# Performance work log

Measured on AMD Instinct MI355X. Metric: run time of the kernel, lower is better.

Reference implementation:

```python
import jax, jax.numpy as jnp
import numpy as np

PATCH_SIZE = 3
CHANNELS = 1
SIGMA_RAW = 0.5
SIGMA_EFF = SIGMA_RAW * PATCH_SIZE ** 2  # sigma * patch_size**2 as in __init__


def setup_inputs() -> dict:
    key = jax.random.key(0)
    kx, ky = jax.random.split(key)
    N, C, H, W = 64, CHANNELS, 64, 64
    x = jax.random.normal(kx, (N, C, H, W), dtype=jnp.float32)
    y = jax.random.normal(ky, (N, C, H, W), dtype=jnp.float32)
    return {"x": x, "y": y}


def _pairwise_patch_distance(A, B):
    # A: (N_A, C, H, W), B: (N_B, C, H, W)
    N_A, C, H, W = A.shape
    N_B = B.shape[0]
    # broadcast pairwise squared pixel diffs: (N_A, N_B, C, H, W)
    pixel_diff = (A[:, None] - B[None]) ** 2
    kern = jnp.ones((1, C, PATCH_SIZE, PATCH_SIZE), dtype=A.dtype)  # OIHW
    d = jax.lax.conv_general_dilated(
        pixel_diff.reshape(N_A * N_B, C, H, W), kern,
        window_strides=(1, 1), padding='VALID',
        dimension_numbers=('NCHW', 'OIHW', 'NCHW'))
    H_new, W_new = d.shape[-2], d.shape[-1]
    return d.reshape(N_A, N_B, H_new, W_new)


def _gaussian_kernel(D):
    return jnp.exp(-D / (2.0 * SIGMA_EFF ** 2))


def _off_mean(K):
    # K: (N, N, h, w); mean over all off-diagonal (i != j) entries
    N, _, h, w = K.shape
    mask = ~jnp.eye(N, dtype=bool)
    total = jnp.sum(jnp.where(mask[:, :, None, None], K, jnp.zeros((), K.dtype)))
    count = (N * (N - 1)) * h * w
    return total / count


def reference(x, y):
    K_xx = _gaussian_kernel(_pairwise_patch_distance(x, x))
    K_xy = _gaussian_kernel(_pairwise_patch_distance(x, y))
    K_yy = _gaussian_kernel(_pairwise_patch_distance(y, y))
    return _off_mean(K_xx) - 2.0 * jnp.mean(K_xy) + _off_mean(K_yy)
```

## Files before the change

### kernel.cpp

```cpp
#include <hip/hip_runtime.h>


typedef __attribute__((ext_vector_type(8))) short short8v;
typedef __attribute__((ext_vector_type(4))) float f32x4;

#define NPOS 3844
#define SIM  196

#if __has_builtin(__builtin_amdgcn_exp2f)
#define EXP2F(v) __builtin_amdgcn_exp2f(v)
#else
#define EXP2F(v) __expf((v) * 0.69314718055994530942f)
#endif

template<int CTRL>
__device__ __forceinline__ float dpp0_f(float v) {
    int r = __builtin_amdgcn_update_dpp(0, __float_as_int(v), CTRL, 0xf, 0xf, true);
    return __int_as_float(r);
}
template<int CTRL, int RM>
__device__ __forceinline__ float dppm_f(float v) {
    int r = __builtin_amdgcn_update_dpp(0, __float_as_int(v), CTRL, RM, 0xf, true);
    return __int_as_float(r);
}
__device__ __forceinline__ float wave_reduce_f(float v) {
    v += dpp0_f<0x111>(v);
    v += dpp0_f<0x112>(v);
    v += dpp0_f<0x114>(v);
    v += dpp0_f<0x118>(v);
    v += dppm_f<0x142, 0xa>(v);
    v += dppm_f<0x143, 0xc>(v);
    return v;
}

__device__ __forceinline__ unsigned int bf16rne(float f) {
    unsigned int u = __float_as_uint(f);
    return (u + 0x7fffu + ((u >> 16) & 1u)) >> 16;
}

__global__ __launch_bounds__(512) void mmd_fused_kernel(
    const float* __restrict__ x, const float* __restrict__ y,
    float* __restrict__ part)
{
    const int t = threadIdx.x, wid = t >> 6, lane = t & 63;
    const int p  = blockIdx.x >> 3;
    const int qg = blockIdx.x & 7;
    const int q  = qg * 8 + wid;

    __shared__ unsigned short stg[128 * SIM];
    __shared__ float pre[8][128];

    #pragma unroll
    for (int u = 0; u < 3; ++u) {
        #pragma unroll
        for (int k = 0; k < 4; ++k) {
            int it = t + k * 512;
            int n = it >> 4, cg = it & 15;
            const float* img = (n < 64) ? (x + n * 4096) : (y + (n - 64) * 4096);
            float4 v = *reinterpret_cast<const float4*>(img + (p + u) * 64 + cg * 4);
            uint2 pk;
            pk.x = bf16rne(v.x) | (bf16rne(v.y) << 16);
            pk.y = bf16rne(v.z) | (bf16rne(v.w) << 16);
            *reinterpret_cast<uint2*>(&stg[n * SIM + u * 64 + cg * 4]) = pk;
        }
    }
    __syncthreads();

    const int r = lane & 15, kg = lane >> 4;
    short8v frag[8];
    #pragma unroll
    for (int g = 0; g < 8; ++g) {
        const unsigned short* bp = &stg[(g * 16 + r) * SIM];
        short8v f = {0, 0, 0, 0, 0, 0, 0, 0};
        if (kg == 0) {
            f[0] = (short)bp[q];
            f[1] = (short)bp[q + 1];
            f[2] = (short)bp[q + 2];
            f[3] = (short)bp[64 + q];
            f[4] = (short)bp[64 + q + 1];
            f[5] = (short)bp[64 + q + 2];
            f[6] = (short)bp[128 + q];
            f[7] = (short)bp[128 + q + 1];
        } else if (kg == 1) {
            f[0] = (short)bp[128 + q + 2];
        }
        frag[g] = f;
    }

    const float NS   = -1.0f / (40.5f * 0.69314718055994530942f);
    const float M2NS = -2.0f * NS;
    const f32x4 zf = {0.f, 0.f, 0.f, 0.f};

    f32x4 accd[8];
    #pragma unroll
    for (int g = 0; g < 8; ++g)
        accd[g] = __builtin_amdgcn_mfma_f32_16x16x32_bf16(frag[g], frag[g], zf, 0, 0, 0);

    const bool holder = ((lane >> 2) & 3) == kg;
    #pragma unroll
    for (int g = 0; g < 8; ++g) {
        float lo = (lane & 1) ? accd[g][1] : accd[g][0];
        float hi = (lane & 1) ? accd[g][3] : accd[g][2];
        float v  = (lane & 2) ? hi : lo;
        if (holder) pre[wid][g * 16 + (lane & 15)] = NS * v;
    }
    __syncthreads();

    float pa[8][4], pb[8];
    #pragma unroll
    for (int g = 0; g < 8; ++g) {
        const float* pp = &pre[wid][g * 16 + kg * 4];
        pa[g][0] = pp[0]; pa[g][1] = pp[1]; pa[g][2] = pp[2]; pa[g][3] = pp[3];
        pb[g] = pre[wid][g * 16 + (lane & 15)];
    }

    float acc_diag = 0.f, acc_same = 0.f, acc_cross = 0.f;

    #pragma unroll
    for (int g = 0; g < 8; ++g)
        #pragma unroll
        for (int m = 0; m < 4; ++m)
            acc_diag += EXP2F(fmaf(accd[g][m], M2NS, pa[g][m] + pb[g]));

    #pragma unroll
    for (int ti = 1; ti < 8; ++ti)
        #pragma unroll
        for (int tj = 0; tj < ti; ++tj) {
            f32x4 c4 = __builtin_amdgcn_mfma_f32_16x16x32_bf16(frag[ti], frag[tj], zf, 0, 0, 0);
            float e = 0.f;
            #pragma unroll
            for (int m = 0; m < 4; ++m)
                e += EXP2F(fmaf(c4[m], M2NS, pa[ti][m] + pb[tj]));
            if (ti >= 4 && tj < 4) acc_cross += e; else acc_same += e;
        }

    acc_diag  = wave_reduce_f(acc_diag);
    acc_same  = wave_reduce_f(acc_same);
    acc_cross = wave_reduce_f(acc_cross);
    if (lane == 63 && q < 62) {
        const int pid = p * 62 + q;
        part[pid]        = acc_diag;
        part[4096 + pid] = acc_same;
        part[8192 + pid] = acc_cross;
    }
}

__global__ __launch_bounds__(1024) void mmd_final_kernel(
    const float* __restrict__ part, float* __restrict__ out)
{
    const int t = threadIdx.x;
    double sd = 0.0, ss = 0.0, sc = 0.0;
    for (int e = t; e < NPOS; e += 1024) {
        sd += (double)part[e];
        ss += (double)part[4096 + e];
        sc += (double)part[8192 + e];
    }
    #pragma unroll
    for (int off = 32; off > 0; off >>= 1) {
        sd += __shfl_xor(sd, off);
        ss += __shfl_xor(ss, off);
        sc += __shfl_xor(sc, off);
    }
    __shared__ double w[3][16];
    const int lane = t & 63, wd = t >> 6;
    if (lane == 0) { w[0][wd] = sd; w[1][wd] = ss; w[2][wd] = sc; }
    __syncthreads();
    if (t == 0) {
        double Sd = 0.0, Ss = 0.0, Sc = 0.0;
        #pragma unroll
        for (int k = 0; k < 16; ++k) { Sd += w[0][k]; Ss += w[1][k]; Sc += w[2][k]; }
        double S_off = (Sd - 128.0 * (double)NPOS) + 2.0 * Ss;
        const double cnt_off = 64.0 * 63.0 * 62.0 * 62.0;
        const double cnt_all = 64.0 * 64.0 * 62.0 * 62.0;
        out[0] = (float)(S_off / cnt_off - 2.0 * Sc / cnt_all);
    }
}

extern "C" void kernel_launch(void* const* d_in, const int* in_sizes, int n_in,
                              void* d_out, int out_size, void* d_ws, size_t ws_size,
                              hipStream_t stream) {
    const float* x = (const float*)d_in[0];
    const float* y = (const float*)d_in[1];
    float* out  = (float*)d_out;
    float* part = (float*)d_ws;

    mmd_fused_kernel<<<62 * 8, 512, 0, stream>>>(x, y, part);
    mmd_final_kernel<<<1, 1024, 0, stream>>>(part, out);
}
```

Measured before the change: 19.11 us.

## Stage narrow per-block windows and prebuilt patch records for vectorized fragment loads

Each block now covers 4 output columns instead of 8, with 256 threads and twice as many blocks. It stages only a 3x8 column window per image instead of three full rows. A second pass packs each 9-pixel patch into a 16-byte record plus a trailing element, so MFMA fragments load with one vector LDS read instead of eight scalar reads. The intent is to cut global loads, shared memory footprint and scalar LDS traffic, and to raise occupancy, at the cost of an extra repacking pass and barrier.

```diff
diff --git a/kernel.cpp b/kernel.cpp
--- a/kernel.cpp
+++ b/kernel.cpp
@@ -5,7 +5,7 @@
 typedef __attribute__((ext_vector_type(4))) float f32x4;
 
 #define NPOS 3844
-#define SIM  196
+#define WSTR 26
 
 #if __has_builtin(__builtin_amdgcn_exp2f)
 #define EXP2F(v) __builtin_amdgcn_exp2f(v)
@@ -32,37 +32,63 @@
     v += dppm_f<0x143, 0xc>(v);
     return v;
 }
-
 __device__ __forceinline__ unsigned int bf16rne(float f) {
     unsigned int u = __float_as_uint(f);
     return (u + 0x7fffu + ((u >> 16) & 1u)) >> 16;
 }
 
-__global__ __launch_bounds__(512) void mmd_fused_kernel(
+__global__ __launch_bounds__(256) void mmd_fused_kernel(
     const float* __restrict__ x, const float* __restrict__ y,
     float* __restrict__ part)
 {
     const int t = threadIdx.x, wid = t >> 6, lane = t & 63;
-    const int p  = blockIdx.x >> 3;
-    const int qg = blockIdx.x & 7;
-    const int q  = qg * 8 + wid;
-
-    __shared__ unsigned short stg[128 * SIM];
-    __shared__ float pre[8][128];
-
-    #pragma unroll
-    for (int u = 0; u < 3; ++u) {
-        #pragma unroll
-        for (int k = 0; k < 4; ++k) {
-            int it = t + k * 512;
-            int n = it >> 4, cg = it & 15;
+    const int p  = blockIdx.x >> 4;
+    const int qg = blockIdx.x & 15;
+    const int q  = qg * 4 + wid;
+
+    __shared__ unsigned short win[128 * WSTR];
+    __shared__ unsigned short rec[4 * 128 * 8];
+    __shared__ unsigned short rec8[4 * 128];
+    __shared__ float pre[4][128];
+
+    {
+        const int cg1 = (qg < 15) ? qg + 1 : 15;
+        #pragma unroll
+        for (int k = 0; k < 3; ++k) {
+            int it = t + k * 256;
+            int n = it / 6, rem = it % 6;
+            int u = rem >> 1, cg = rem & 1;
             const float* img = (n < 64) ? (x + n * 4096) : (y + (n - 64) * 4096);
-            float4 v = *reinterpret_cast<const float4*>(img + (p + u) * 64 + cg * 4);
-            uint2 pk;
-            pk.x = bf16rne(v.x) | (bf16rne(v.y) << 16);
-            pk.y = bf16rne(v.z) | (bf16rne(v.w) << 16);
-            *reinterpret_cast<uint2*>(&stg[n * SIM + u * 64 + cg * 4]) = pk;
+            float4 v = *reinterpret_cast<const float4*>(
+                img + (p + u) * 64 + ((cg ? cg1 : qg) << 2));
+            unsigned int d0 = bf16rne(v.x) | (bf16rne(v.y) << 16);
+            unsigned int d1 = bf16rne(v.z) | (bf16rne(v.w) << 16);
+            unsigned int* w32 = reinterpret_cast<unsigned int*>(
+                &win[n * WSTR + u * 8 + cg * 4]);
+            w32[0] = d0; w32[1] = d1;
         }
+    }
+    __syncthreads();
+
+    #pragma unroll
+    for (int k = 0; k < 2; ++k) {
+        int rid = t + k * 256;
+        int ql = rid >> 7, n = rid & 127;
+        const unsigned short* wp = &win[n * WSTR + ql];
+        unsigned short b[9];
+        #pragma unroll
+        for (int u = 0; u < 3; ++u) {
+            b[u * 3 + 0] = wp[u * 8 + 0];
+            b[u * 3 + 1] = wp[u * 8 + 1];
+            b[u * 3 + 2] = wp[u * 8 + 2];
+        }
+        uint4 pk;
+        pk.x = b[0] | ((unsigned)b[1] << 16);
+        pk.y = b[2] | ((unsigned)b[3] << 16);
+        pk.z = b[4] | ((unsigned)b[5] << 16);
+        pk.w = b[6] | ((unsigned)b[7] << 16);
+        *reinterpret_cast<uint4*>(&rec[(size_t)rid * 8]) = pk;
+        rec8[rid] = b[8];
     }
     __syncthreads();
 
@@ -70,20 +96,11 @@
     short8v frag[8];
     #pragma unroll
     for (int g = 0; g < 8; ++g) {
-        const unsigned short* bp = &stg[(g * 16 + r) * SIM];
         short8v f = {0, 0, 0, 0, 0, 0, 0, 0};
-        if (kg == 0) {
-            f[0] = (short)bp[q];
-            f[1] = (short)bp[q + 1];
-            f[2] = (short)bp[q + 2];
-            f[3] = (short)bp[64 + q];
-            f[4] = (short)bp[64 + q + 1];
-            f[5] = (short)bp[64 + q + 2];
-            f[6] = (short)bp[128 + q];
-            f[7] = (short)bp[128 + q + 1];
-        } else if (kg == 1) {
-            f[0] = (short)bp[128 + q + 2];
-        }
+        if (kg == 0)
+            f = *reinterpret_cast<const short8v*>(&rec[(size_t)(wid * 128 + g * 16 + r) * 8]);
+        else if (kg == 1)
+            f[0] = (short)rec8[wid * 128 + g * 16 + r];
         frag[g] = f;
     }
 
@@ -184,6 +201,6 @@
     float* out  = (float*)d_out;
     float* part = (float*)d_ws;
 
-    mmd_fused_kernel<<<62 * 8, 512, 0, stream>>>(x, y, part);
+    mmd_fused_kernel<<<62 * 16, 256, 0, stream>>>(x, y, part);
     mmd_final_kernel<<<1, 1024, 0, stream>>>(part, out);
 }
```

After: 20.28 us. +6.1%, slower.
